# Kernel tuning notes

Hardware: AMD Instinct MI355X
Metric: run time of the kernel (lower is better)

Reference implementation:

```python
import jax, jax.numpy as jnp
import numpy as np

LATENT = 512
CIN = 512
COUT = 512
K = 3
B, H, W = 16, 64, 64

# equalized-lr multipliers (use_wscale=True, lrmul=1, gain=1)
W_MUL_CONV = (CIN * K * K) ** (-0.5)
W_MUL_DENSE = LATENT ** (-0.5)


def setup_inputs() -> dict:
    key = jax.random.key(0)
    k1, k2, k3, k4 = jax.random.split(key, 4)
    x = jax.random.normal(k1, (B, CIN, H, W), dtype=jnp.float32)
    y = jax.random.normal(k2, (B, LATENT), dtype=jnp.float32)
    dense_w = jax.random.normal(k3, (CIN, LATENT), dtype=jnp.float32)
    dense_b = jnp.ones((CIN,), dtype=jnp.float32)  # style bias, init 1 (StyleGAN2)
    weight = jax.random.normal(k4, (COUT, CIN, K, K), dtype=jnp.float32)
    return {"x": x, "y": y, "dense_w": dense_w, "dense_b": dense_b, "weight": weight}


def reference(x, y, dense_w, dense_b, weight):
    # style: s[b, cin] = (y @ dense_w.T) * w_mul + bias (linear bias_act)
    s = jnp.einsum('bl,cl->bc', y, dense_w) * W_MUL_DENSE + dense_b  # [B, Cin]

    # modulate: per-sample weights ww[b,o,i,kh,kw]
    w = weight * W_MUL_CONV
    ww = w[None] * s[:, None, :, None, None]  # [B, Cout, Cin, K, K]

    # demodulate
    d = jax.lax.rsqrt(jnp.sum(ww * ww, axis=(2, 3, 4)) + 1e-8)  # [B, Cout]
    ww = ww * d[:, :, None, None, None]

    # fused grouped conv: groups = B, VALID padding (F.conv2d default)
    b = x.shape[0]
    x_g = x.reshape(1, b * CIN, H, W)
    w_g = ww.reshape(b * COUT, CIN, K, K)
    out = jax.lax.conv_general_dilated(
        x_g, w_g,
        window_strides=(1, 1), padding='VALID',
        dimension_numbers=('NCHW', 'OIHW', 'NCHW'),
        feature_group_count=b)
    return out.reshape(b, COUT, H - K + 1, W - K + 1)
```

## Files before the change

kernel.cpp:

```cpp
#include <hip/hip_runtime.h>
#include <hip/hip_bf16.h>

#define CIN 512
#define COUT 512
#define BATCH 16
#define NP 3844
#define OW 62

#define W_MUL_DENSE 0.044194173824159216f
#define W_MUL_CONV  0.014731391274719736f

using short8  = __attribute__((ext_vector_type(8))) short;
using floatx4 = __attribute__((ext_vector_type(4))) float;
using uintx4  = __attribute__((ext_vector_type(4))) unsigned int;

__device__ __forceinline__ unsigned short f2bfu(float f) {
    unsigned u = __builtin_bit_cast(unsigned, f);
    u += 0x7FFFu + ((u >> 16) & 1u);
    return (unsigned short)(u >> 16);
}


__global__ void emc_style_kernel(const float* __restrict__ y, const float* __restrict__ dw,
                                 const float* __restrict__ db, float* __restrict__ s) {
    int idx = blockIdx.x * 256 + threadIdx.x;
    int b = idx >> 9, c = idx & 511;
    const float4* yb = (const float4*)(y + b * 512);
    const float4* wc = (const float4*)(dw + c * 512);
    float acc = 0.f;
#pragma unroll 4
    for (int l = 0; l < 128; ++l) {
        float4 a = yb[l], w4 = wc[l];
        acc += a.x * w4.x + a.y * w4.y + a.z * w4.z + a.w * w4.w;
    }
    s[idx] = acc * W_MUL_DENSE + db[c];
}

__global__ void emc_wsq_kernel(const float* __restrict__ w, float* __restrict__ wsq) {
    int idx = blockIdx.x * 256 + threadIdx.x;
    const float* p = w + (size_t)idx * 9;
    float a = 0.f;
#pragma unroll
    for (int j = 0; j < 9; ++j) a += p[j] * p[j];
    wsq[idx] = a;
}

__global__ void emc_demod_kernel(const float* __restrict__ s, const float* __restrict__ wsq,
                                 float* __restrict__ d) {
    int idx = blockIdx.x * 256 + threadIdx.x;
    int b = idx >> 9, o = idx & 511;
    const float4* sb = (const float4*)(s + b * 512);
    const float4* wo = (const float4*)(wsq + o * 512);
    float acc = 0.f;
#pragma unroll 4
    for (int l = 0; l < 128; ++l) {
        float4 a = sb[l], c = wo[l];
        acc += a.x * a.x * c.x + a.y * a.y * c.y + a.z * a.z * c.z + a.w * a.w * c.w;
    }
    d[idx] = rsqrtf(W_MUL_CONV * W_MUL_CONV * acc + 1e-8f);
}

__global__ void emc_wrepack_kernel(const float* __restrict__ w, unsigned short* __restrict__ wb) {
    int idx = blockIdx.x * 256 + threadIdx.x;
    int i = idx & 511;
    int r = idx >> 9;
    int kpos = r % 9;
    int o = r / 9;
    wb[idx] = f2bfu(w[(size_t)(o * 512 + i) * 9 + kpos]);
}


__global__ __launch_bounds__(256, 2) void emc_conv_kernel(
    const float* __restrict__ x, const unsigned short* __restrict__ wb,
    const float* __restrict__ sv, const float* __restrict__ dv,
    float* __restrict__ out) {

    __shared__ __align__(16) unsigned short smB[260 * 40];
    __shared__ float s_s[512];
    __shared__ float s_d[256];

    int orig = blockIdx.x;
    int cpx = gridDim.x >> 3;
    int bid = (orig & 7) * cpx + (orig >> 3);

    int b = bid / 62;
    int t = bid - b * 62;
    int ot = t & 1;
    int strip = t >> 1;
    int oB = ot * 256;
    int r0 = strip * 2;

    int tid = threadIdx.x;
    int lane = tid & 63;
    int wid = tid >> 6;

    s_s[tid]       = sv[b * 512 + tid];
    s_s[tid + 256] = sv[b * 512 + 256 + tid];
    s_d[tid]       = dv[b * 512 + oB + tid];

    int sc = tid & 63;
    int sr = tid >> 6;
    const float* xrow = x + (size_t)b * (512 * 4096) + (r0 + sr) * 64 + sc;
    unsigned short* bg = smB + (sr * 64 + sc) * 40;

    int frc = lane & 15, q = lane >> 4;

    int voffA[4];
#pragma unroll
    for (int m = 0; m < 4; ++m)
        voffA[m] = (wid * 64 + m * 16 + frc) * 9216 + q * 16;

    int bidx[8];
#pragma unroll
    for (int n = 0; n < 8; ++n) bidx[n] = (n * 16 + frc) * 40 + q * 8;

    floatx4 acc[4][8];
#pragma unroll
    for (int m = 0; m < 4; ++m)
#pragma unroll
        for (int n = 0; n < 8; ++n) acc[m][n] = floatx4{0.f, 0.f, 0.f, 0.f};

    short8 fA0[4], fA1[4];
    float raw[8];
    unsigned held[16];

    const char* wbB = (const char*)wb + (size_t)oB * 9216;

    auto AISSUE = [&](int it, int kN, short8* dst) {
        const char* abase = wbB + (kN * 512 + it * 32) * 2;
#pragma unroll
        for (int m = 0; m < 4; ++m)
            dst[m] = *(const short8*)(abase + voffA[m]);
    };

    auto LOAD_SLICE = [&](int itgt, int sl) {
        const float* xp = xrow + ((size_t)itgt * 32 + sl * 4) * 4096;
        int r = (sl & 1) * 4;
        raw[r + 0] = xp[0];
        raw[r + 1] = xp[4096];
        raw[r + 2] = xp[2 * 4096];
        raw[r + 3] = xp[3 * 4096];
    };

    auto CONVERT = [&](int itgt, int sl) {
        int i0 = itgt * 32 + sl * 4;
        int r = (sl & 1) * 4;
        float v0 = raw[r + 0] * s_s[i0];
        float v1 = raw[r + 1] * s_s[i0 + 1];
        float v2 = raw[r + 2] * s_s[i0 + 2];
        float v3 = raw[r + 3] * s_s[i0 + 3];
        held[2 * sl]     = (unsigned)f2bfu(v0) | ((unsigned)f2bfu(v1) << 16);
        held[2 * sl + 1] = (unsigned)f2bfu(v2) | ((unsigned)f2bfu(v3) << 16);
    };

    auto WRITE_B = [&]() {
        *(uintx4*)(bg)      = uintx4{held[0],  held[1],  held[2],  held[3]};
        *(uintx4*)(bg + 8)  = uintx4{held[4],  held[5],  held[6],  held[7]};
        *(uintx4*)(bg + 16) = uintx4{held[8],  held[9],  held[10], held[11]};
        *(uintx4*)(bg + 24) = uintx4{held[12], held[13], held[14], held[15]};
    };

    auto MFMA32 = [&](int kpos, short8* fc) {
        int kh = kpos / 3, kw = kpos - kh * 3;
        int bo = (kh * 64 + kw) * 40;
        short8 bfr[8];
#pragma unroll
        for (int n = 0; n < 8; ++n) bfr[n] = *(const short8*)(smB + bidx[n] + bo);
        __builtin_amdgcn_s_setprio(1);
#pragma unroll
        for (int m = 0; m < 4; ++m)
#pragma unroll
            for (int n = 0; n < 8; ++n)
                acc[m][n] = __builtin_amdgcn_mfma_f32_16x16x32_bf16(
                    fc[m], bfr[n], acc[m][n], 0, 0, 0);
        __builtin_amdgcn_s_setprio(0);
    };

    auto PHASE = [&](int it, int kpos, int par, bool stage, bool issueNext) {
        short8* fc = par ? fA1 : fA0;
        if (stage && kpos < 8) LOAD_SLICE(it + 1, kpos);
        if (stage && kpos >= 1) CONVERT(it + 1, kpos - 1);
        MFMA32(kpos, fc);
        if (issueNext) {
            int iN = (kpos >= 7) ? it + 1 : it;
            int kN = (kpos + 2) % 9;
            AISSUE(iN, kN, fc);
        }
        if (stage && kpos == 8) {
            __builtin_amdgcn_s_barrier();
            WRITE_B();
            asm volatile("s_waitcnt lgkmcnt(0)" ::: "memory");
            __builtin_amdgcn_s_barrier();
        }
    };

    __syncthreads();

    AISSUE(0, 0, fA0);
    AISSUE(0, 1, fA1);
#pragma unroll
    for (int sl = 0; sl < 8; ++sl) {
        LOAD_SLICE(0, sl);
        if (sl > 0) CONVERT(0, sl - 1);
    }
    CONVERT(0, 7);
    WRITE_B();
    __syncthreads();

    for (int itp = 0; itp < 7; ++itp) {
        int ite = itp * 2, ito = itp * 2 + 1;
#pragma unroll
        for (int k = 0; k < 9; ++k) PHASE(ite, k, k & 1, true, true);
#pragma unroll
        for (int k = 0; k < 9; ++k) PHASE(ito, k, (k + 1) & 1, true, true);
    }
#pragma unroll
    for (int k = 0; k < 9; ++k) PHASE(14, k, k & 1, true, true);
#pragma unroll
    for (int k = 0; k < 9; ++k) PHASE(15, k, (k + 1) & 1, false, k <= 6);

    size_t outb = (size_t)b * 512 * NP;
#pragma unroll
    for (int m = 0; m < 4; ++m) {
#pragma unroll
        for (int r = 0; r < 4; ++r) {
            int o_l = wid * 64 + m * 16 + q * 4 + r;
            float scale = W_MUL_CONV * s_d[o_l];
            size_t rb = outb + (size_t)(oB + o_l) * NP + strip * 124;
#pragma unroll
            for (int n = 0; n < 8; ++n) {
                int row = n >> 2;
                int col = (n & 3) * 16 + frc;
                if (col < OW) out[rb + row * OW + col] = acc[m][n][r] * scale;
            }
        }
    }
}

extern "C" void kernel_launch(void* const* d_in, const int* in_sizes, int n_in,
                              void* d_out, int out_size, void* d_ws, size_t ws_size,
                              hipStream_t stream) {
    const float* x  = (const float*)d_in[0];
    const float* y  = (const float*)d_in[1];
    const float* dw = (const float*)d_in[2];
    const float* db = (const float*)d_in[3];
    const float* w  = (const float*)d_in[4];
    float* out = (float*)d_out;

    char* ws = (char*)d_ws;
    float* s_  = (float*)ws;
    float* d_  = (float*)(ws + 32768);
    float* wsq = (float*)(ws + 65536);
    unsigned short* wb = (unsigned short*)(ws + 65536 + 1048576);

    emc_style_kernel<<<32, 256, 0, stream>>>(y, dw, db, s_);
    emc_wsq_kernel<<<1024, 256, 0, stream>>>(w, wsq);
    emc_demod_kernel<<<32, 256, 0, stream>>>(s_, wsq, d_);
    emc_wrepack_kernel<<<9216, 256, 0, stream>>>(w, wb);
    emc_conv_kernel<<<16 * 62, 256, 0, stream>>>(x, wb, s_, d_, out);
}
```

Before: 384.0 us.

## Split conv tile across 8 waves with 2x2 wave grid and single A buffer

The conv kernel moves from 256 to 512 threads per block. Waves are arranged as 4 row groups by 2 column groups, so each wave owns a 64x64 accumulator tile instead of 64x128. Staging of the x tile is split between the two thread halves, and the double-buffered A fragments become a single buffer reloaded after each MFMA group. This halves per-wave register pressure so more waves can be resident, at the cost of more redundant A loads per block and less latency hiding on the A prefetch.

```diff
diff --git a/kernel.cpp b/kernel.cpp
--- a/kernel.cpp
+++ b/kernel.cpp
@@ -70,7 +70,7 @@
 }
 
 
-__global__ __launch_bounds__(256, 2) void emc_conv_kernel(
+__global__ __launch_bounds__(512, 4) void emc_conv_kernel(
     const float* __restrict__ x, const unsigned short* __restrict__ wb,
     const float* __restrict__ sv, const float* __restrict__ dv,
     float* __restrict__ out) {
@@ -94,110 +94,82 @@
     int lane = tid & 63;
     int wid = tid >> 6;
 
-    s_s[tid]       = sv[b * 512 + tid];
-    s_s[tid + 256] = sv[b * 512 + 256 + tid];
-    s_d[tid]       = dv[b * 512 + oB + tid];
+    s_s[tid & 511] = sv[b * 512 + (tid & 511)];
+    if (tid < 256) s_d[tid] = dv[b * 512 + oB + tid];
 
     int sc = tid & 63;
-    int sr = tid >> 6;
-    const float* xrow = x + (size_t)b * (512 * 4096) + (r0 + sr) * 64 + sc;
-    unsigned short* bg = smB + (sr * 64 + sc) * 40;
+    int sr = (tid >> 6) & 3;
+    int h  = tid >> 8;
+    const float* xrow = x + (size_t)b * (512 * 4096) + (r0 + sr) * 64 + sc + (size_t)h * 16 * 4096;
+    unsigned short* bg = smB + (sr * 64 + sc) * 40 + h * 16;
 
     int frc = lane & 15, q = lane >> 4;
-
+    int wr = wid >> 1, wc = wid & 1;
+
+    const char* wbB = (const char*)wb + (size_t)oB * 9216;
     int voffA[4];
 #pragma unroll
     for (int m = 0; m < 4; ++m)
-        voffA[m] = (wid * 64 + m * 16 + frc) * 9216 + q * 16;
-
-    int bidx[8];
-#pragma unroll
-    for (int n = 0; n < 8; ++n) bidx[n] = (n * 16 + frc) * 40 + q * 8;
-
-    floatx4 acc[4][8];
+        voffA[m] = (wr * 64 + m * 16 + frc) * 9216 + q * 16;
+
+    int bidx0 = (wc * 64 + frc) * 40 + q * 8;
+
+    floatx4 acc[4][4];
 #pragma unroll
     for (int m = 0; m < 4; ++m)
 #pragma unroll
-        for (int n = 0; n < 8; ++n) acc[m][n] = floatx4{0.f, 0.f, 0.f, 0.f};
-
-    short8 fA0[4], fA1[4];
-    float raw[8];
-    unsigned held[16];
-
-    const char* wbB = (const char*)wb + (size_t)oB * 9216;
-
-    auto AISSUE = [&](int it, int kN, short8* dst) {
-        const char* abase = wbB + (kN * 512 + it * 32) * 2;
+        for (int n = 0; n < 4; ++n) acc[m][n] = floatx4{0.f, 0.f, 0.f, 0.f};
+
+    short8 fA[4];
+    float raw[4];
+    unsigned held[8];
+
+    auto AISSUE = [&](int it, int kN) {
+        const char* abase = wbB + (size_t)(kN * 512 + it * 32) * 2;
 #pragma unroll
         for (int m = 0; m < 4; ++m)
-            dst[m] = *(const short8*)(abase + voffA[m]);
+            fA[m] = *(const short8*)(abase + voffA[m]);
     };
 
     auto LOAD_SLICE = [&](int itgt, int sl) {
-        const float* xp = xrow + ((size_t)itgt * 32 + sl * 4) * 4096;
-        int r = (sl & 1) * 4;
+        const float* xp = xrow + ((size_t)itgt * 32 + sl * 2) * 4096;
+        int r = (sl & 1) * 2;
         raw[r + 0] = xp[0];
         raw[r + 1] = xp[4096];
-        raw[r + 2] = xp[2 * 4096];
-        raw[r + 3] = xp[3 * 4096];
     };
 
     auto CONVERT = [&](int itgt, int sl) {
-        int i0 = itgt * 32 + sl * 4;
-        int r = (sl & 1) * 4;
+        int i0 = itgt * 32 + h * 16 + sl * 2;
+        int r = (sl & 1) * 2;
         float v0 = raw[r + 0] * s_s[i0];
         float v1 = raw[r + 1] * s_s[i0 + 1];
-        float v2 = raw[r + 2] * s_s[i0 + 2];
-        float v3 = raw[r + 3] * s_s[i0 + 3];
-        held[2 * sl]     = (unsigned)f2bfu(v0) | ((unsigned)f2bfu(v1) << 16);
-        held[2 * sl + 1] = (unsigned)f2bfu(v2) | ((unsigned)f2bfu(v3) << 16);
+        held[sl] = (unsigned)f2bfu(v0) | ((unsigned)f2bfu(v1) << 16);
     };
 
     auto WRITE_B = [&]() {
-        *(uintx4*)(bg)      = uintx4{held[0],  held[1],  held[2],  held[3]};
-        *(uintx4*)(bg + 8)  = uintx4{held[4],  held[5],  held[6],  held[7]};
-        *(uintx4*)(bg + 16) = uintx4{held[8],  held[9],  held[10], held[11]};
-        *(uintx4*)(bg + 24) = uintx4{held[12], held[13], held[14], held[15]};
-    };
-
-    auto MFMA32 = [&](int kpos, short8* fc) {
+        *(uintx4*)(bg)     = uintx4{held[0], held[1], held[2], held[3]};
+        *(uintx4*)(bg + 8) = uintx4{held[4], held[5], held[6], held[7]};
+    };
+
+    auto MFMA16 = [&](int kpos) {
         int kh = kpos / 3, kw = kpos - kh * 3;
         int bo = (kh * 64 + kw) * 40;
-        short8 bfr[8];
-#pragma unroll
-        for (int n = 0; n < 8; ++n) bfr[n] = *(const short8*)(smB + bidx[n] + bo);
+        short8 bfr[4];
+#pragma unroll
+        for (int n = 0; n < 4; ++n) bfr[n] = *(const short8*)(smB + bidx0 + bo + n * 640);
         __builtin_amdgcn_s_setprio(1);
 #pragma unroll
         for (int m = 0; m < 4; ++m)
 #pragma unroll
-            for (int n = 0; n < 8; ++n)
+            for (int n = 0; n < 4; ++n)
                 acc[m][n] = __builtin_amdgcn_mfma_f32_16x16x32_bf16(
-                    fc[m], bfr[n], acc[m][n], 0, 0, 0);
+                    fA[m], bfr[n], acc[m][n], 0, 0, 0);
         __builtin_amdgcn_s_setprio(0);
     };
 
-    auto PHASE = [&](int it, int kpos, int par, bool stage, bool issueNext) {
-        short8* fc = par ? fA1 : fA0;
-        if (stage && kpos < 8) LOAD_SLICE(it + 1, kpos);
-        if (stage && kpos >= 1) CONVERT(it + 1, kpos - 1);
-        MFMA32(kpos, fc);
-        if (issueNext) {
-            int iN = (kpos >= 7) ? it + 1 : it;
-            int kN = (kpos + 2) % 9;
-            AISSUE(iN, kN, fc);
-        }
-        if (stage && kpos == 8) {
-            __builtin_amdgcn_s_barrier();
-            WRITE_B();
-            asm volatile("s_waitcnt lgkmcnt(0)" ::: "memory");
-            __builtin_amdgcn_s_barrier();
-        }
-    };
-
     __syncthreads();
 
-    AISSUE(0, 0, fA0);
-    AISSUE(0, 1, fA1);
+    AISSUE(0, 0);
 #pragma unroll
     for (int sl = 0; sl < 8; ++sl) {
         LOAD_SLICE(0, sl);
@@ -207,31 +179,41 @@
     WRITE_B();
     __syncthreads();
 
-    for (int itp = 0; itp < 7; ++itp) {
-        int ite = itp * 2, ito = itp * 2 + 1;
-#pragma unroll
-        for (int k = 0; k < 9; ++k) PHASE(ite, k, k & 1, true, true);
-#pragma unroll
-        for (int k = 0; k < 9; ++k) PHASE(ito, k, (k + 1) & 1, true, true);
-    }
-#pragma unroll
-    for (int k = 0; k < 9; ++k) PHASE(14, k, k & 1, true, true);
-#pragma unroll
-    for (int k = 0; k < 9; ++k) PHASE(15, k, (k + 1) & 1, false, k <= 6);
+    for (int itile = 0; itile < 15; ++itile) {
+#pragma unroll
+        for (int kpos = 0; kpos < 9; ++kpos) {
+            if (kpos < 8) LOAD_SLICE(itile + 1, kpos);
+            if (kpos >= 1) CONVERT(itile + 1, kpos - 1);
+            MFMA16(kpos);
+            if (kpos < 8) {
+                AISSUE(itile, kpos + 1);
+            } else {
+                AISSUE(itile + 1, 0);
+                __builtin_amdgcn_s_barrier();
+                WRITE_B();
+                asm volatile("s_waitcnt lgkmcnt(0)" ::: "memory");
+                __builtin_amdgcn_s_barrier();
+            }
+        }
+    }
+#pragma unroll
+    for (int kpos = 0; kpos < 9; ++kpos) {
+        MFMA16(kpos);
+        if (kpos < 8) AISSUE(15, kpos + 1);
+    }
 
     size_t outb = (size_t)b * 512 * NP;
 #pragma unroll
     for (int m = 0; m < 4; ++m) {
 #pragma unroll
         for (int r = 0; r < 4; ++r) {
-            int o_l = wid * 64 + m * 16 + q * 4 + r;
+            int o_l = wr * 64 + m * 16 + q * 4 + r;
             float scale = W_MUL_CONV * s_d[o_l];
-            size_t rb = outb + (size_t)(oB + o_l) * NP + strip * 124;
-#pragma unroll
-            for (int n = 0; n < 8; ++n) {
-                int row = n >> 2;
-                int col = (n & 3) * 16 + frc;
-                if (col < OW) out[rb + row * OW + col] = acc[m][n][r] * scale;
+            size_t rb = outb + (size_t)(oB + o_l) * NP + strip * 124 + wc * OW;
+#pragma unroll
+            for (int n = 0; n < 4; ++n) {
+                int col = n * 16 + frc;
+                if (col < OW) out[rb + col] = acc[m][n][r] * scale;
             }
         }
     }
@@ -257,5 +239,5 @@
     emc_wsq_kernel<<<1024, 256, 0, stream>>>(w, wsq);
     emc_demod_kernel<<<32, 256, 0, stream>>>(s_, wsq, d_);
     emc_wrepack_kernel<<<9216, 256, 0, stream>>>(w, wb);
-    emc_conv_kernel<<<16 * 62, 256, 0, stream>>>(x, wb, s_, d_, out);
-}
+    emc_conv_kernel<<<16 * 62, 512, 0, stream>>>(x, wb, s_, d_, out);
+}
```

Result: slower. 845.8 us (+120.3%).
